# Optimization experiments

Hardware: AMD Instinct MI355X
Metric: run time of the kernel (lower is better)

## Reference

```python
import jax, jax.numpy as jnp
import numpy as np


def setup_inputs() -> dict:
    key = jax.random.key(0)
    # [batch, heads, seq, head_dim]
    hidden_states = jax.random.normal(key, (2, 16, 2048, 64), dtype=jnp.float32)
    return {"hidden_states": hidden_states}


def reference(hidden_states):
    q = k = v = hidden_states
    # scores: [b, h, s, s] -- note: NO 1/sqrt(d) scaling, matching the original.
    scores = jnp.einsum("bhqd,bhkd->bhqk", q, k)
    a = jax.nn.softmax(scores, axis=-1)
    out = jnp.einsum("bhqk,bhkd->bhqd", a, v)
    return out
```

## Files before the change

### kernel.cpp

```cpp
#include <hip/hip_runtime.h>
#include <hip/hip_bf16.h>
#include <stdint.h>


typedef __bf16 bf16x8 __attribute__((ext_vector_type(8)));
typedef __bf16 bf16x4 __attribute__((ext_vector_type(4)));
typedef __bf16 bf16x2 __attribute__((ext_vector_type(2)));
typedef float f32x4 __attribute__((ext_vector_type(4)));
typedef float f32x16 __attribute__((ext_vector_type(16)));
typedef unsigned int u32x4v __attribute__((ext_vector_type(4)));

#define SEQ 2048
#define HD 64
#define KVB 64
#define NBH 32
#define NTILE (SEQ / KVB)
#define IMG_BYTES 8192
#define PAIR_BYTES 16384
#define IMG_TOT ((size_t)NBH * NTILE * PAIR_BYTES)
#define WS_IMG IMG_TOT

#define QPB 128

__device__ __forceinline__ int swz(int row, int byteoff) {
    return byteoff ^ ((row & 7) << 4);
}

__device__ __forceinline__ float fexp2(float x) {
    float r;
    asm("v_exp_f32 %0, %1" : "=v"(r) : "v"(x));
    return r;
}

__device__ __forceinline__ unsigned pk_bf16(float a, float b) {
    bf16x2 v;
    v[0] = (__bf16)a;
    v[1] = (__bf16)b;
    return __builtin_bit_cast(unsigned, v);
}

__device__ __forceinline__ bf16x8 read_frag8(const char* base, int r, int p0) {
    const char* rowp = base + r * 128;
    const int rr = r & 15;
    bf16x4 lo = *(const bf16x4*)(rowp + (((p0 + 0) ^ rr) << 3));
    bf16x4 hi4 = *(const bf16x4*)(rowp + (((p0 + 1) ^ rr) << 3));
    bf16x8 f;
    f[0] = lo[0]; f[1] = lo[1]; f[2] = lo[2]; f[3] = lo[3];
    f[4] = hi4[0]; f[5] = hi4[1]; f[6] = hi4[2]; f[7] = hi4[3];
    return f;
}

#if __has_builtin(__builtin_amdgcn_global_load_lds)
#define HAVE_GLLDS 1
typedef const __attribute__((address_space(1))) unsigned int* gas_t;
typedef __attribute__((address_space(3))) unsigned int* las_t;
__device__ __forceinline__ void gl_lds16(const void* g, void* l) {
    __builtin_amdgcn_global_load_lds((gas_t)g, (las_t)l, 16, 0, 0);
}
#else
#define HAVE_GLLDS 0
#endif

__global__ __launch_bounds__(256)
void prep_kernel(const float* __restrict__ x, char* __restrict__ ws) {
    const int bh = blockIdx.y;
    const int tile = blockIdx.x;
    const int kv0 = tile * KVB;
    const int t = threadIdx.x;
    const int srow = t >> 2;
    const int scq = (t & 3) * 16;
    const float* __restrict__ X = x + (size_t)bh * SEQ * HD;
    char* __restrict__ img = ws + ((size_t)bh * NTILE + tile) * PAIR_BYTES;

    const int rr = srow & 15;
    const int p = scq >> 2;

    {
        const float* src = X + (size_t)(kv0 + srow) * HD + scq;
        float4 a = *(const float4*)(src);
        float4 b = *(const float4*)(src + 4);
        float4 c = *(const float4*)(src + 8);
        float4 d = *(const float4*)(src + 12);
        bf16x4 k0, k1, k2, k3;
        k0[0] = (__bf16)a.x; k0[1] = (__bf16)a.y; k0[2] = (__bf16)a.z; k0[3] = (__bf16)a.w;
        k1[0] = (__bf16)b.x; k1[1] = (__bf16)b.y; k1[2] = (__bf16)b.z; k1[3] = (__bf16)b.w;
        k2[0] = (__bf16)c.x; k2[1] = (__bf16)c.y; k2[2] = (__bf16)c.z; k2[3] = (__bf16)c.w;
        k3[0] = (__bf16)d.x; k3[1] = (__bf16)d.y; k3[2] = (__bf16)d.z; k3[3] = (__bf16)d.w;
        char* rowp = img + srow * 128;
        *(bf16x4*)(rowp + (((p + 0) ^ rr) << 3)) = k0;
        *(bf16x4*)(rowp + (((p + 1) ^ rr) << 3)) = k1;
        *(bf16x4*)(rowp + (((p + 2) ^ rr) << 3)) = k2;
        *(bf16x4*)(rowp + (((p + 3) ^ rr) << 3)) = k3;
    }
    {
        bf16x4 g0, g1, g2, g3;
#pragma unroll
        for (int j = 0; j < 4; ++j) {
            g0[j] = (__bf16)X[(size_t)(kv0 + scq + j) * HD + srow];
            g1[j] = (__bf16)X[(size_t)(kv0 + scq + 4 + j) * HD + srow];
            g2[j] = (__bf16)X[(size_t)(kv0 + scq + 8 + j) * HD + srow];
            g3[j] = (__bf16)X[(size_t)(kv0 + scq + 12 + j) * HD + srow];
        }
        char* rowp = img + IMG_BYTES + srow * 128;
        *(bf16x4*)(rowp + (((p + 0) ^ rr) << 3)) = g0;
        *(bf16x4*)(rowp + (((p + 1) ^ rr) << 3)) = g1;
        *(bf16x4*)(rowp + (((p + 2) ^ rr) << 3)) = g2;
        *(bf16x4*)(rowp + (((p + 3) ^ rr) << 3)) = g3;
    }
}

__global__ __launch_bounds__(256, 4)
void attn_img_kernel(const float* __restrict__ x, const char* __restrict__ ws,
                     float* __restrict__ outp) {
    __shared__ __align__(16) char kbuf[2][IMG_BYTES];
    __shared__ __align__(16) char vbuf[2][IMG_BYTES];

    const int wg = blockIdx.x;
    const int sid = (wg & 7) * 64 + (wg >> 3);
    const int bh = sid >> 4;
    const int q0 = (sid & 15) * QPB;

    const float* __restrict__ X = x + (size_t)bh * SEQ * HD;
    const char* __restrict__ wsb = ws + (size_t)bh * NTILE * PAIR_BYTES;

    const int t = threadIdx.x;
    const int wave = t >> 6;
    const int lane = t & 63;
    const int ln = lane & 31;
    const int hi = lane >> 5;

    const int qbase = q0 + wave * 32;

    const float SCL = 1.4426950408889634f;
    bf16x8 qf[4];
    float m = 0.f;
    {
        const float* qsrc = X + (size_t)(qbase + ln) * HD;
#pragma unroll
        for (int j = 0; j < 16; ++j) {
            float4 v = *(const float4*)(qsrc + j * 4);
            m += v.x * v.x + v.y * v.y + v.z * v.z + v.w * v.w;
        }
        m *= SCL;
#pragma unroll
        for (int dt = 0; dt < 4; ++dt) {
            const float* s8 = qsrc + dt * 16 + hi * 8;
            float4 a = *(const float4*)s8;
            float4 b = *(const float4*)(s8 + 4);
            bf16x8 f;
            f[0] = (__bf16)(a.x * SCL); f[1] = (__bf16)(a.y * SCL);
            f[2] = (__bf16)(a.z * SCL); f[3] = (__bf16)(a.w * SCL);
            f[4] = (__bf16)(b.x * SCL); f[5] = (__bf16)(b.y * SCL);
            f[6] = (__bf16)(b.z * SCL); f[7] = (__bf16)(b.w * SCL);
            qf[dt] = f;
        }
    }
    const float negm = -m;

    bf16x8 onef;
    {
        u32x4v w;
        w[0] = 0x3F803F80u; w[1] = 0x3F803F80u; w[2] = 0x3F803F80u; w[3] = 0x3F803F80u;
        onef = __builtin_bit_cast(bf16x8, w);
    }

    f32x16 acc0, acc1, lac;
#pragma unroll
    for (int i = 0; i < 16; ++i) { acc0[i] = 0.f; acc1[i] = 0.f; lac[i] = 0.f; }

#if HAVE_GLLDS
    {
        char* base = (wave & 2) ? &vbuf[0][(wave & 1) * 4096] : &kbuf[0][(wave & 1) * 4096];
        const char* sp = wsb + wave * 4096 + lane * 16;
#pragma unroll
        for (int j = 0; j < 4; ++j)
            gl_lds16(sp + j * 1024, base + j * 1024);
    }
#else
    {
        const char* img = wsb;
#pragma unroll
        for (int q = 0; q < 4; ++q) {
            bf16x8 d0 = *(const bf16x8*)(img + q * 4096 + t * 16);
            char* dst = (q & 2) ? &vbuf[0][(q & 1) * 4096] : &kbuf[0][(q & 1) * 4096];
            *(bf16x8*)&dst[t * 16] = d0;
        }
    }
#endif
    __syncthreads();

    for (int it = 0; it < NTILE; ++it) {
        const int cur = it & 1;

#if HAVE_GLLDS
        if (it + 1 < NTILE) {
            const char* img = wsb + (size_t)(it + 1) * PAIR_BYTES;
            char* base = (wave & 2) ? &vbuf[cur ^ 1][(wave & 1) * 4096]
                                    : &kbuf[cur ^ 1][(wave & 1) * 4096];
            const char* sp = img + wave * 4096 + lane * 16;
#pragma unroll
            for (int j = 0; j < 4; ++j)
                gl_lds16(sp + j * 1024, base + j * 1024);
        }
#else
        bf16x8 n0, n1, n2, n3;
        if (it + 1 < NTILE) {
            const char* img = wsb + (size_t)(it + 1) * PAIR_BYTES;
            n0 = *(const bf16x8*)(img + t * 16);
            n1 = *(const bf16x8*)(img + 4096 + t * 16);
            n2 = *(const bf16x8*)(img + 8192 + t * 16);
            n3 = *(const bf16x8*)(img + 12288 + t * 16);
        }
#endif

        const char* kb = kbuf[cur];
        const char* vb = vbuf[cur];

        f32x16 s0, s1;
#pragma unroll
        for (int i = 0; i < 16; ++i) { s0[i] = negm; s1[i] = negm; }
        __builtin_amdgcn_s_setprio(1);
#pragma unroll
        for (int dt = 0; dt < 4; ++dt) {
            const int p0 = dt * 4 + hi * 2;
            bf16x8 kf0 = read_frag8(kb, ln, p0);
            s0 = __builtin_amdgcn_mfma_f32_32x32x16_bf16(kf0, qf[dt], s0, 0, 0, 0);
            bf16x8 kf1 = read_frag8(kb, 32 + ln, p0);
            s1 = __builtin_amdgcn_mfma_f32_32x32x16_bf16(kf1, qf[dt], s1, 0, 0, 0);
        }
        __builtin_amdgcn_s_setprio(0);

        f32x16 e0, e1;
#pragma unroll
        for (int i = 0; i < 16; ++i) {
            e0[i] = fexp2(s0[i]);
            e1[i] = fexp2(s1[i]);
        }

        bf16x8 pa[4];
#pragma unroll
        for (int kt = 0; kt < 4; ++kt) {
            const f32x16& e = (kt & 2) ? e1 : e0;
            const int sx = 8 * (kt & 1);
            unsigned wA = pk_bf16(e[sx + 0], e[sx + 1]);
            unsigned wB = pk_bf16(e[sx + 2], e[sx + 3]);
            unsigned wC = pk_bf16(e[sx + 4], e[sx + 5]);
            unsigned wD = pk_bf16(e[sx + 6], e[sx + 7]);
            asm("v_permlane32_swap_b32 %0, %1" : "+v"(wA), "+v"(wC));
            asm("v_permlane32_swap_b32 %0, %1" : "+v"(wB), "+v"(wD));
            u32x4v w;
            w[0] = wA; w[1] = wB; w[2] = wC; w[3] = wD;
            pa[kt] = __builtin_bit_cast(bf16x8, w);
        }

        __builtin_amdgcn_s_setprio(1);
#pragma unroll
        for (int kt = 0; kt < 4; ++kt) {
            const int p0 = kt * 4 + hi * 2;
            bf16x8 vf0 = read_frag8(vb, ln, p0);
            acc0 = __builtin_amdgcn_mfma_f32_32x32x16_bf16(pa[kt], vf0, acc0, 0, 0, 0);
            bf16x8 vf1 = read_frag8(vb, 32 + ln, p0);
            acc1 = __builtin_amdgcn_mfma_f32_32x32x16_bf16(pa[kt], vf1, acc1, 0, 0, 0);
            lac = __builtin_amdgcn_mfma_f32_32x32x16_bf16(pa[kt], onef, lac, 0, 0, 0);
        }
        __builtin_amdgcn_s_setprio(0);

#if !HAVE_GLLDS
        if (it + 1 < NTILE) {
            const int nxt = cur ^ 1;
            *(bf16x8*)&kbuf[nxt][t * 16] = n0;
            *(bf16x8*)&kbuf[nxt][4096 + t * 16] = n1;
            *(bf16x8*)&vbuf[nxt][t * 16] = n2;
            *(bf16x8*)&vbuf[nxt][4096 + t * 16] = n3;
        }
#endif
        __syncthreads();
    }

    float* Op = outp + (size_t)bh * SEQ * HD;
#pragma unroll
    for (int r = 0; r < 16; ++r) {
        const int qr = (r & 3) + 8 * (r >> 2) + 4 * hi;
        const float il = 1.f / lac[r];
        float* dst = Op + (size_t)(qbase + qr) * HD + ln;
        dst[0]  = acc0[r] * il;
        dst[32] = acc1[r] * il;
    }
}

__global__ __launch_bounds__(256, 2)
void attn_fwd_kernel(const float* __restrict__ x, float* __restrict__ out) {
    __shared__ __align__(16) char k_lds[KVB * HD * 2];
    __shared__ __align__(16) char vt_lds[HD * KVB * 2];
    __shared__ __align__(16) char p_lds2[4][2][16 * KVB * 2];

    const int bh = blockIdx.y;
    const int q0 = blockIdx.x * 128;
    const float* __restrict__ X = x + (size_t)bh * SEQ * HD;
    float* __restrict__ Op = out + (size_t)bh * SEQ * HD;

    const int t = threadIdx.x;
    const int wave = t >> 6;
    const int lane = t & 63;
    const int lgrp = lane >> 4;
    const int lid = lane & 15;

    bf16x8 qf[2][2];
#pragma unroll
    for (int rt = 0; rt < 2; ++rt) {
        const int row = q0 + wave * 32 + rt * 16 + lid;
#pragma unroll
        for (int kc = 0; kc < 2; ++kc) {
            const float* src = X + (size_t)row * HD + kc * 32 + lgrp * 8;
            float4 a = *(const float4*)src;
            float4 b = *(const float4*)(src + 4);
            bf16x8 f;
            f[0] = (__bf16)a.x; f[1] = (__bf16)a.y; f[2] = (__bf16)a.z; f[3] = (__bf16)a.w;
            f[4] = (__bf16)b.x; f[5] = (__bf16)b.y; f[6] = (__bf16)b.z; f[7] = (__bf16)b.w;
            qf[rt][kc] = f;
        }
    }

    f32x4 acc[2][4];
    float m[2][4], l[2][4];
#pragma unroll
    for (int rt = 0; rt < 2; ++rt)
#pragma unroll
        for (int i = 0; i < 4; ++i) {
            acc[rt][i][0] = 0.f; acc[rt][i][1] = 0.f;
            acc[rt][i][2] = 0.f; acc[rt][i][3] = 0.f;
            m[rt][i] = -1e30f;
            l[rt][i] = 0.f;
        }

    const int srow = t >> 2;
    const int scq = (t & 3) * 16;

    for (int kv0 = 0; kv0 < SEQ; kv0 += KVB) {
        {
            const float* src = X + (size_t)(kv0 + srow) * HD + scq;
            float4 a = *(const float4*)(src);
            float4 b = *(const float4*)(src + 4);
            float4 c = *(const float4*)(src + 8);
            float4 d = *(const float4*)(src + 12);
            bf16x8 f0, f1;
            f0[0] = (__bf16)a.x; f0[1] = (__bf16)a.y; f0[2] = (__bf16)a.z; f0[3] = (__bf16)a.w;
            f0[4] = (__bf16)b.x; f0[5] = (__bf16)b.y; f0[6] = (__bf16)b.z; f0[7] = (__bf16)b.w;
            f1[0] = (__bf16)c.x; f1[1] = (__bf16)c.y; f1[2] = (__bf16)c.z; f1[3] = (__bf16)c.w;
            f1[4] = (__bf16)d.x; f1[5] = (__bf16)d.y; f1[6] = (__bf16)d.z; f1[7] = (__bf16)d.w;
            *(bf16x8*)&k_lds[swz(srow, srow * 128 + scq * 2)] = f0;
            *(bf16x8*)&k_lds[swz(srow, srow * 128 + scq * 2 + 16)] = f1;
        }
        {
            bf16x8 g0, g1;
#pragma unroll
            for (int j = 0; j < 8; ++j)
                g0[j] = (__bf16)X[(size_t)(kv0 + scq + j) * HD + srow];
#pragma unroll
            for (int j = 0; j < 8; ++j)
                g1[j] = (__bf16)X[(size_t)(kv0 + scq + 8 + j) * HD + srow];
            *(bf16x8*)&vt_lds[swz(srow, srow * 128 + scq * 2)] = g0;
            *(bf16x8*)&vt_lds[swz(srow, srow * 128 + scq * 2 + 16)] = g1;
        }
        __syncthreads();

#pragma unroll
        for (int rt = 0; rt < 2; ++rt) {
            f32x4 s[4];
#pragma unroll
            for (int kt = 0; kt < 4; ++kt) {
                f32x4 z = {0.f, 0.f, 0.f, 0.f};
#pragma unroll
                for (int kc = 0; kc < 2; ++kc) {
                    const int krow = kt * 16 + lid;
                    bf16x8 kfr = *(const bf16x8*)&k_lds[swz(krow, krow * 128 + (kc * 32 + lgrp * 8) * 2)];
                    z = __builtin_amdgcn_mfma_f32_16x16x32_bf16(qf[rt][kc], kfr, z, 0, 0, 0);
                }
                s[kt] = z;
            }

            char* pl = p_lds2[wave][rt];
#pragma unroll
            for (int r = 0; r < 4; ++r) {
                float mxv = fmaxf(fmaxf(s[0][r], s[1][r]), fmaxf(s[2][r], s[3][r]));
                mxv = fmaxf(mxv, __shfl_xor(mxv, 1));
                mxv = fmaxf(mxv, __shfl_xor(mxv, 2));
                mxv = fmaxf(mxv, __shfl_xor(mxv, 4));
                mxv = fmaxf(mxv, __shfl_xor(mxv, 8));
                const float mold = m[rt][r];
                const float mnew = fmaxf(mold, mxv);
                const float alpha = __expf(mold - mnew);
                const int prow = lgrp * 4 + r;
                float psum = 0.f;
#pragma unroll
                for (int kt = 0; kt < 4; ++kt) {
                    float p = __expf(s[kt][r] - mnew);
                    psum += p;
                    *(__bf16*)&pl[swz(prow, prow * 128 + (kt * 16 + lid) * 2)] = (__bf16)p;
                }
                psum += __shfl_xor(psum, 1);
                psum += __shfl_xor(psum, 2);
                psum += __shfl_xor(psum, 4);
                psum += __shfl_xor(psum, 8);
                l[rt][r] = l[rt][r] * alpha + psum;
                m[rt][r] = mnew;
#pragma unroll
                for (int ct = 0; ct < 4; ++ct)
                    acc[rt][ct][r] *= alpha;
            }

#pragma unroll
            for (int kc = 0; kc < 2; ++kc) {
                bf16x8 pfr = *(const bf16x8*)&pl[swz(lid, lid * 128 + (kc * 32 + lgrp * 8) * 2)];
#pragma unroll
                for (int ct = 0; ct < 4; ++ct) {
                    const int vrow = ct * 16 + lid;
                    bf16x8 vf = *(const bf16x8*)&vt_lds[swz(vrow, vrow * 128 + (kc * 32 + lgrp * 8) * 2)];
                    acc[rt][ct] = __builtin_amdgcn_mfma_f32_16x16x32_bf16(pfr, vf, acc[rt][ct], 0, 0, 0);
                }
            }
        }
        __syncthreads();
    }

#pragma unroll
    for (int rt = 0; rt < 2; ++rt)
#pragma unroll
        for (int r = 0; r < 4; ++r) {
            const float inv = 1.f / l[rt][r];
            const int row = q0 + wave * 32 + rt * 16 + lgrp * 4 + r;
            float* dst = Op + (size_t)row * HD + lid;
#pragma unroll
            for (int ct = 0; ct < 4; ++ct)
                dst[ct * 16] = acc[rt][ct][r] * inv;
        }
}

extern "C" void kernel_launch(void* const* d_in, const int* in_sizes, int n_in,
                              void* d_out, int out_size, void* d_ws, size_t ws_size,
                              hipStream_t stream) {
    const float* x = (const float*)d_in[0];
    float* out = (float*)d_out;
    char* ws = (char*)d_ws;
    if (ws_size >= WS_IMG) {
        dim3 pgrid(NTILE, NBH);
        hipLaunchKernelGGL(prep_kernel, pgrid, dim3(256), 0, stream, x, ws);
        hipLaunchKernelGGL(attn_img_kernel, dim3(512), dim3(256), 0, stream,
                           x, ws, out);
    } else {
        dim3 grid(SEQ / 128, NBH);
        hipLaunchKernelGGL(attn_fwd_kernel, grid, dim3(256), 0, stream, x, out);
    }
}
```

Before: 85.63 us.

## Triple-buffer K/V tiles with split barrier and compute row sums on VALU

Replaces the double-buffered K/V LDS tiles with a three-slot ring filled by direct global-to-LDS loads two tiles ahead. Each iteration waits on vmcnt and uses a plain s_barrier instead of a full __syncthreads, so loads overlap with compute more deeply. The softmax denominator is now accumulated with VALU adds and a cross-half shuffle instead of an extra MFMA against a ones vector. The max subtraction moves from the score accumulator's initial value into the exp argument. The extra LDS slot lowers the occupancy hint from 4 to 2 blocks per CU.

```diff
diff --git a/kernel.cpp b/kernel.cpp
--- a/kernel.cpp
+++ b/kernel.cpp
@@ -109,11 +109,14 @@
     }
 }
 
-__global__ __launch_bounds__(256, 4)
+__global__ __launch_bounds__(256, 2)
 void attn_img_kernel(const float* __restrict__ x, const char* __restrict__ ws,
                      float* __restrict__ outp) {
-    __shared__ __align__(16) char kbuf[2][IMG_BYTES];
-    __shared__ __align__(16) char vbuf[2][IMG_BYTES];
+#if HAVE_GLLDS
+    __shared__ __align__(16) char lds3[3][PAIR_BYTES];
+#else
+    __shared__ __align__(16) char lds3[2][PAIR_BYTES];
+#endif
 
     const int wg = blockIdx.x;
     const int sid = (wg & 7) * 64 + (wg >> 3);
@@ -130,6 +133,19 @@
     const int hi = lane >> 5;
 
     const int qbase = q0 + wave * 32;
+
+#if HAVE_GLLDS
+    {
+        const char* sp0 = wsb + wave * 4096 + lane * 16;
+#pragma unroll
+        for (int j = 0; j < 4; ++j)
+            gl_lds16(sp0 + j * 1024, &lds3[0][wave * 4096 + j * 1024] + lane * 16);
+        const char* sp1 = wsb + PAIR_BYTES + wave * 4096 + lane * 16;
+#pragma unroll
+        for (int j = 0; j < 4; ++j)
+            gl_lds16(sp1 + j * 1024, &lds3[1][wave * 4096 + j * 1024] + lane * 16);
+    }
+#endif
 
     const float SCL = 1.4426950408889634f;
     bf16x8 qf[4];
@@ -155,53 +171,43 @@
             qf[dt] = f;
         }
     }
-    const float negm = -m;
-
-    bf16x8 onef;
-    {
-        u32x4v w;
-        w[0] = 0x3F803F80u; w[1] = 0x3F803F80u; w[2] = 0x3F803F80u; w[3] = 0x3F803F80u;
-        onef = __builtin_bit_cast(bf16x8, w);
-    }
-
-    f32x16 acc0, acc1, lac;
-#pragma unroll
-    for (int i = 0; i < 16; ++i) { acc0[i] = 0.f; acc1[i] = 0.f; lac[i] = 0.f; }
-
-#if HAVE_GLLDS
-    {
-        char* base = (wave & 2) ? &vbuf[0][(wave & 1) * 4096] : &kbuf[0][(wave & 1) * 4096];
-        const char* sp = wsb + wave * 4096 + lane * 16;
-#pragma unroll
-        for (int j = 0; j < 4; ++j)
-            gl_lds16(sp + j * 1024, base + j * 1024);
-    }
-#else
+
+    f32x16 acc0, acc1;
+#pragma unroll
+    for (int i = 0; i < 16; ++i) { acc0[i] = 0.f; acc1[i] = 0.f; }
+    float l = 0.f;
+
+#if !HAVE_GLLDS
     {
         const char* img = wsb;
 #pragma unroll
         for (int q = 0; q < 4; ++q) {
             bf16x8 d0 = *(const bf16x8*)(img + q * 4096 + t * 16);
-            char* dst = (q & 2) ? &vbuf[0][(q & 1) * 4096] : &kbuf[0][(q & 1) * 4096];
-            *(bf16x8*)&dst[t * 16] = d0;
-        }
-    }
-#endif
+            *(bf16x8*)&lds3[0][q * 4096 + t * 16] = d0;
+        }
+    }
     __syncthreads();
+#endif
 
     for (int it = 0; it < NTILE; ++it) {
-        const int cur = it & 1;
-
 #if HAVE_GLLDS
         if (it + 1 < NTILE) {
-            const char* img = wsb + (size_t)(it + 1) * PAIR_BYTES;
-            char* base = (wave & 2) ? &vbuf[cur ^ 1][(wave & 1) * 4096]
-                                    : &kbuf[cur ^ 1][(wave & 1) * 4096];
+            asm volatile("s_waitcnt vmcnt(4)" ::: "memory");
+        } else {
+            asm volatile("s_waitcnt vmcnt(0)" ::: "memory");
+        }
+        __builtin_amdgcn_s_barrier();
+        __builtin_amdgcn_sched_barrier(0);
+
+        if (it + 2 < NTILE) {
+            const char* img = wsb + (size_t)(it + 2) * PAIR_BYTES;
+            char* dst = &lds3[(it + 2) % 3][wave * 4096] + lane * 16;
             const char* sp = img + wave * 4096 + lane * 16;
 #pragma unroll
             for (int j = 0; j < 4; ++j)
-                gl_lds16(sp + j * 1024, base + j * 1024);
-        }
+                gl_lds16(sp + j * 1024, dst + j * 1024);
+        }
+        const char* kb = lds3[it % 3];
 #else
         bf16x8 n0, n1, n2, n3;
         if (it + 1 < NTILE) {
@@ -211,14 +217,13 @@
             n2 = *(const bf16x8*)(img + 8192 + t * 16);
             n3 = *(const bf16x8*)(img + 12288 + t * 16);
         }
-#endif
-
-        const char* kb = kbuf[cur];
-        const char* vb = vbuf[cur];
+        const char* kb = lds3[it & 1];
+#endif
+        const char* vb = kb + IMG_BYTES;
 
         f32x16 s0, s1;
 #pragma unroll
-        for (int i = 0; i < 16; ++i) { s0[i] = negm; s1[i] = negm; }
+        for (int i = 0; i < 16; ++i) { s0[i] = 0.f; s1[i] = 0.f; }
         __builtin_amdgcn_s_setprio(1);
 #pragma unroll
         for (int dt = 0; dt < 4; ++dt) {
@@ -233,9 +238,14 @@
         f32x16 e0, e1;
 #pragma unroll
         for (int i = 0; i < 16; ++i) {
-            e0[i] = fexp2(s0[i]);
-            e1[i] = fexp2(s1[i]);
-        }
+            e0[i] = fexp2(s0[i] - m);
+            e1[i] = fexp2(s1[i] - m);
+        }
+        float ps = 0.f;
+#pragma unroll
+        for (int i = 0; i < 16; ++i) ps += e0[i] + e1[i];
+        ps += __shfl_xor(ps, 32);
+        l += ps;
 
         bf16x8 pa[4];
 #pragma unroll
@@ -261,27 +271,28 @@
             acc0 = __builtin_amdgcn_mfma_f32_32x32x16_bf16(pa[kt], vf0, acc0, 0, 0, 0);
             bf16x8 vf1 = read_frag8(vb, 32 + ln, p0);
             acc1 = __builtin_amdgcn_mfma_f32_32x32x16_bf16(pa[kt], vf1, acc1, 0, 0, 0);
-            lac = __builtin_amdgcn_mfma_f32_32x32x16_bf16(pa[kt], onef, lac, 0, 0, 0);
         }
         __builtin_amdgcn_s_setprio(0);
 
 #if !HAVE_GLLDS
         if (it + 1 < NTILE) {
-            const int nxt = cur ^ 1;
-            *(bf16x8*)&kbuf[nxt][t * 16] = n0;
-            *(bf16x8*)&kbuf[nxt][4096 + t * 16] = n1;
-            *(bf16x8*)&vbuf[nxt][t * 16] = n2;
-            *(bf16x8*)&vbuf[nxt][4096 + t * 16] = n3;
-        }
-#endif
-        __syncthreads();
+            const int nxt = (it + 1) & 1;
+            __syncthreads();
+            *(bf16x8*)&lds3[nxt][t * 16] = n0;
+            *(bf16x8*)&lds3[nxt][4096 + t * 16] = n1;
+            *(bf16x8*)&lds3[nxt][8192 + t * 16] = n2;
+            *(bf16x8*)&lds3[nxt][12288 + t * 16] = n3;
+            __syncthreads();
+        }
+#endif
     }
 
     float* Op = outp + (size_t)bh * SEQ * HD;
+    const float invl = 1.f / l;
 #pragma unroll
     for (int r = 0; r < 16; ++r) {
         const int qr = (r & 3) + 8 * (r >> 2) + 4 * hi;
-        const float il = 1.f / lac[r];
+        const float il = __shfl(invl, qr);
         float* dst = Op + (size_t)(qbase + qr) * HD + ln;
         dst[0]  = acc0[r] * il;
         dst[32] = acc1[r] * il;
```

Measured after the change: 71.10 us. -17.0%, faster.
